# Kernel tuning notes

Hardware: AMD Instinct MI355X
Metric: run time of the kernel (lower is better)

The kernel has to match this reference:

```python
import jax, jax.numpy as jnp
import numpy as np

B, S, D = 1, 2048, 2048
HQ, HKV = 32, 8
HD = D // HQ          # 64
G = HQ // HKV         # 4 query heads per kv head


def apply_rope(x, freq):
    # x: (b, h, s, hd); freq: (s, hd//2) angles. Llama-style pairwise rotation.
    cos = jnp.cos(freq)  # (s, hd//2)
    sin = jnp.sin(freq)
    xr = x.reshape(*x.shape[:-1], HD // 2, 2)
    xe, xo = xr[..., 0], xr[..., 1]
    re = xe * cos - xo * sin
    ro = xe * sin + xo * cos
    return jnp.stack([re, ro], axis=-1).reshape(x.shape)


def setup_inputs() -> dict:
    key = jax.random.key(0)
    k1, k2, k3, k4, k5 = jax.random.split(key, 5)
    x = jax.random.normal(k1, (B, S, D), dtype=jnp.float32)
    # RoPE angles: pos * inv_freq, theta=10000
    inv_freq = 1.0 / (10000.0 ** (jnp.arange(0, HD, 2, dtype=jnp.float32) / HD))
    freq = jnp.arange(S, dtype=jnp.float32)[:, None] * inv_freq[None, :]  # (S, HD//2)
    mask = jnp.tril(jnp.ones((S, S), dtype=jnp.int32))
    scale = D ** -0.5
    wq = jax.random.normal(k2, (D, HQ * HD), dtype=jnp.float32) * scale
    wk = jax.random.normal(k3, (D, HKV * HD), dtype=jnp.float32) * scale
    wv = jax.random.normal(k4, (D, HKV * HD), dtype=jnp.float32) * scale
    wo = jax.random.normal(k5, (HQ * HD, D), dtype=jnp.float32) * scale
    return {"x": x, "freq": freq, "mask": mask, "wq": wq, "wk": wk, "wv": wv, "wo": wo}


def reference(x, freq, mask, wq, wk, wv, wo):
    b, s, d = x.shape
    q = (x @ wq).reshape(b, s, HQ, HD).transpose(0, 2, 1, 3)    # (b,HQ,s,hd)
    k = (x @ wk).reshape(b, s, HKV, HD).transpose(0, 2, 1, 3)   # (b,HKV,s,hd)
    v = (x @ wv).reshape(b, s, HKV, HD).transpose(0, 2, 1, 3)
    q = apply_rope(q, freq[:s])
    k = apply_rope(k, freq[:s])
    # GQA: broadcast kv heads over groups instead of repeat_interleave
    qg = q.reshape(b, HKV, G, s, HD)
    scores = jnp.einsum('bhgsd,bhtd->bhgst', qg, k)             # (b,HKV,G,s,s)
    scores = jnp.where(mask[:s, :s] == 0, -jnp.inf, scores)
    w = jax.nn.softmax(scores * (HD ** -0.5), axis=-1)
    out = jnp.einsum('bhgst,bhtd->bhgsd', w, v)
    out = out.reshape(b, HQ, s, HD).transpose(0, 2, 1, 3).reshape(b, s, HQ * HD)
    return out @ wo
```

## Files before the change

### kernel.cpp

```cpp
#include <hip/hip_runtime.h>

typedef unsigned short u16;
typedef unsigned int u32;
typedef unsigned long long u64;

using bf16x8 = __bf16 __attribute__((ext_vector_type(8)));
using f32x4  = float  __attribute__((ext_vector_type(4)));

#define LDS_SPACE __attribute__((address_space(3)))
#define GLB_SPACE __attribute__((address_space(1)))

static __device__ __forceinline__ u16 f2bf(float f) {
  union { float f; u32 u; } c; c.f = f;
  u32 u = c.u;
  return (u16)((u + 0x7fffu + ((u >> 16) & 1u)) >> 16);
}
static __device__ __forceinline__ float bf2f(u16 u) {
  union { u32 u; float f; } c; c.u = ((u32)u) << 16;
  return c.f;
}

static __device__ __forceinline__ void fence_barrier() {
  asm volatile("" ::: "memory");
  __builtin_amdgcn_s_barrier();
  asm volatile("" ::: "memory");
}

constexpr float SC = 0.18033688011112042f;

__global__ __launch_bounds__(256) void prep_k(const float* __restrict__ x,
                                              const float* __restrict__ wq,
                                              const float* __restrict__ wk,
                                              const float* __restrict__ wv,
                                              const float* __restrict__ wo,
                                              u16* __restrict__ x_bf,
                                              u16* __restrict__ wqkv_t,
                                              u16* __restrict__ wo_t) {
  const int b = blockIdx.x;
  if (b < 4096) {
    int i = b * 256 + threadIdx.x;
    float4 v = ((const float4*)x)[i];
    ushort4 o;
    o.x = f2bf(v.x); o.y = f2bf(v.y); o.z = f2bf(v.z); o.w = f2bf(v.w);
    ((ushort4*)x_bf)[i] = o;
    return;
  }
  const float* src; u16* dst; int C, bx, by; float scale = 1.0f;
  if (b < 8192)      { src = wq; dst = wqkv_t; C = 2048; int t = b - 4096; bx = t & 63; by = t >> 6; scale = SC; }
  else if (b < 9216) { src = wk; dst = wqkv_t + (size_t)2048 * 2048; C = 512; int t = b - 8192; bx = t & 15; by = t >> 4; }
  else if (b < 10240){ src = wv; dst = wqkv_t + (size_t)2560 * 2048; C = 512; int t = b - 9216; bx = t & 15; by = t >> 4; }
  else               { src = wo; dst = wo_t; C = 2048; int t = b - 10240; bx = t & 63; by = t >> 6; }
  __shared__ float t[32][33];
  const int lx = threadIdx.x & 31, ly = threadIdx.x >> 5;
  const int r0 = by * 32, c0 = bx * 32;
  #pragma unroll
  for (int i = 0; i < 32; i += 8)
    t[ly + i][lx] = src[(size_t)(r0 + ly + i) * C + c0 + lx];
  __syncthreads();
  #pragma unroll
  for (int i = 0; i < 32; i += 8)
    dst[(size_t)(c0 + ly + i) * 2048 + r0 + lx] = f2bf(t[lx][ly + i] * scale);
}

__global__ __launch_bounds__(256) void vtrans_k(const u16* __restrict__ Y,
                                                u16* __restrict__ Vt) {
  __shared__ u16 t[64][72];
  const int s0 = blockIdx.x * 64;
  const int c0 = blockIdx.y * 64;
  const int lx = threadIdx.x & 63, ly = threadIdx.x >> 6;
  #pragma unroll
  for (int i = 0; i < 64; i += 4)
    t[i + ly][lx] = Y[(size_t)(s0 + i + ly) * 3072 + 2560 + c0 + lx];
  __syncthreads();
  #pragma unroll
  for (int i = 0; i < 64; i += 4)
    Vt[(size_t)(c0 + i + ly) * 2048 + s0 + lx] = t[lx][i + ly];
}

template <typename OutT>
__global__ __launch_bounds__(256) void gemm64_k(const u16* __restrict__ A,
                                                const u16* __restrict__ Bt,
                                                OutT* __restrict__ C,
                                                int M, int N, int K) {
  __shared__ u16 As[2][64 * 64];
  __shared__ u16 Bs[2][128 * 64];
  const int tid = threadIdx.x, lane = tid & 63, w = tid >> 6;
  const int wr = w >> 1, wc = w & 1;
  const int bm = blockIdx.y, bn = blockIdx.x;
  const int l15 = lane & 15, lq = lane >> 4;
  f32x4 acc[2][4] = {};

  const int srow8 = lane >> 3;
  const int scolb = ((lane & 7) ^ srow8) * 16;
  const u16* AgR = A + (size_t)(bm * 64 + w * 16 + srow8) * K;
  const u16* BgR = Bt + (size_t)(bn * 128 + w * 32 + srow8) * K;

  auto stage = [&](int buf, int k0) {
    #pragma unroll
    for (int i = 0; i < 2; ++i)
      __builtin_amdgcn_global_load_lds(
          (const GLB_SPACE u32*)((const char*)(AgR + (size_t)i * 8 * K + k0) + scolb),
          (LDS_SPACE u32*)&As[buf][(w * 16 + i * 8) * 64], 16, 0, 0);
    #pragma unroll
    for (int i = 0; i < 4; ++i)
      __builtin_amdgcn_global_load_lds(
          (const GLB_SPACE u32*)((const char*)(BgR + (size_t)i * 8 * K + k0) + scolb),
          (LDS_SPACE u32*)&Bs[buf][(w * 32 + i * 8) * 64], 16, 0, 0);
  };

  stage(0, 0);
  for (int k0 = 0; k0 < K; k0 += 64) {
    const int cur = (k0 >> 6) & 1;
    fence_barrier();
    if (k0 + 64 < K) {
      stage(cur ^ 1, k0 + 64);
      asm volatile("s_waitcnt vmcnt(6)" ::: "memory");
    } else {
      asm volatile("s_waitcnt vmcnt(0)" ::: "memory");
    }
    fence_barrier();

    #pragma unroll
    for (int kk = 0; kk < 2; ++kk) {
      bf16x8 a[2], b[4];
      #pragma unroll
      for (int m = 0; m < 2; ++m) {
        const int ra = wr * 32 + m * 16 + l15;
        a[m] = *(const bf16x8*)&As[cur][ra * 64 + (((kk * 4 + lq) ^ (ra & 7)) << 3)];
      }
      #pragma unroll
      for (int n = 0; n < 4; ++n) {
        const int rb = wc * 64 + n * 16 + l15;
        b[n] = *(const bf16x8*)&Bs[cur][rb * 64 + (((kk * 4 + lq) ^ (rb & 7)) << 3)];
      }
      #pragma unroll
      for (int m = 0; m < 2; ++m)
        #pragma unroll
        for (int n = 0; n < 4; ++n)
          acc[m][n] = __builtin_amdgcn_mfma_f32_16x16x32_bf16(a[m], b[n], acc[m][n], 0, 0, 0);
    }
  }

  const int r0 = bm * 64 + wr * 32 + lq * 4;
  const int c0 = bn * 128 + wc * 64 + l15;
  #pragma unroll
  for (int m = 0; m < 2; ++m)
    #pragma unroll
    for (int n = 0; n < 4; ++n)
      #pragma unroll
      for (int r = 0; r < 4; ++r) {
        float v = acc[m][n][r];
        size_t off = (size_t)(r0 + m * 16 + r) * N + (c0 + n * 16);
        if constexpr (sizeof(OutT) == 2) ((u16*)C)[off] = f2bf(v);
        else C[off] = v;
      }
}

__global__ __launch_bounds__(256) void rope_k(u16* __restrict__ Y,
                                              const float* __restrict__ freq) {
  int idx = blockIdx.x * 256 + threadIdx.x;
  int s = idx / 1280;
  int rem = idx - s * 1280;
  int h = rem >> 5;
  int i = rem & 31;
  int col = (h < 32) ? (h * 64 + 2 * i) : (2048 + (h - 32) * 64 + 2 * i);
  float ang = freq[s * 32 + i];
  float sn, cs;
  sincosf(ang, &sn, &cs);
  size_t base = (size_t)s * 3072 + col;
  float e = bf2f(Y[base]), o = bf2f(Y[base + 1]);
  Y[base]     = f2bf(e * cs - o * sn);
  Y[base + 1] = f2bf(e * sn + o * cs);
}

__global__ __launch_bounds__(256, 3) void attn_part_k(const u16* __restrict__ Y,
                                                      const u16* __restrict__ Vtg,
                                                      u16* __restrict__ Opart,
                                                      float2* __restrict__ Ml,
                                                      u16* __restrict__ Out) {
  __shared__ u16 Ks[2][64 * 64];
  __shared__ u16 Vs[2][64 * 64];
  __shared__ u32 Ps[4][2][16 * 36];
  const int w = threadIdx.x >> 6, lane = threadIdx.x & 63;
  const int l15 = lane & 15, lq = lane >> 4;

  const int b = (int)blockIdx.x;
  const int head = b & 31;
  const int idx = b >> 5;
  const u64 tb = (idx < 12) ? 986161012810415591ULL : 1200400570313029ULL;
  const int v = (int)((tb >> ((idx < 12 ? idx : idx - 12) * 5)) & 31);
  const int qt = v & 15, ch = v >> 4;
  const int kvh = head >> 2;
  const int ntiles = 2 * qt + 2;
  const int half = qt + 1;
  const int tstart = ch ? half : 0;
  const int tend = (qt >= 8 && ch == 0) ? half : ntiles;
  const int q0w = qt * 128 + w * 32;

  const int srow = lane >> 3;
  const int scolb = ((lane & 7) ^ srow) * 16;
  auto stage = [&](int buf, int t) {
    const int t0 = t * 64;
    #pragma unroll
    for (int i = 0; i < 2; ++i) {
      const int r = w * 16 + i * 8;
      const char* gk = (const char*)(Y + (size_t)(t0 + r + srow) * 3072 + 2048 + kvh * 64) + scolb;
      __builtin_amdgcn_global_load_lds((const GLB_SPACE u32*)gk,
                                       (LDS_SPACE u32*)&Ks[buf][r * 64], 16, 0, 0);
      const char* gv = (const char*)(Vtg + (size_t)(kvh * 64 + r + srow) * 2048 + t0) + scolb;
      __builtin_amdgcn_global_load_lds((const GLB_SPACE u32*)gv,
                                       (LDS_SPACE u32*)&Vs[buf][r * 64], 16, 0, 0);
    }
  };

  stage(0, tstart);

  bf16x8 qf[2][2];
  #pragma unroll
  for (int qs = 0; qs < 2; ++qs)
    #pragma unroll
    for (int kk = 0; kk < 2; ++kk)
      qf[qs][kk] = *(const bf16x8*)&Y[(size_t)(q0w + qs * 16 + l15) * 3072 +
                                      head * 64 + kk * 32 + lq * 8];

  float m_[2] = { -1e30f, -1e30f };
  float l_[2] = { 0.f, 0.f };
  f32x4 accO[2][4] = {};

  for (int t = tstart; t < tend; ++t) {
    const int cur = (t - tstart) & 1;
    fence_barrier();
    if (t + 1 < tend) {
      stage(cur ^ 1, t + 1);
      asm volatile("s_waitcnt vmcnt(4)" ::: "memory");
    } else {
      asm volatile("s_waitcnt vmcnt(0)" ::: "memory");
    }
    fence_barrier();

    const int t0 = t * 64;
    if (t0 > q0w + 31) continue;

    const u16* Kb = Ks[cur];
    const u16* Vb = Vs[cur];

    f32x4 sc[2][4] = {};
    #pragma unroll
    for (int kk = 0; kk < 2; ++kk)
      #pragma unroll
      for (int kt = 0; kt < 4; ++kt) {
        const int rk = kt * 16 + l15;
        bf16x8 a = *(const bf16x8*)&Kb[rk * 64 + ((((kk * 4 + lq) ^ (rk & 7)) << 3))];
        sc[0][kt] = __builtin_amdgcn_mfma_f32_16x16x32_bf16(a, qf[0][kk], sc[0][kt], 0, 0, 0);
        sc[1][kt] = __builtin_amdgcn_mfma_f32_16x16x32_bf16(a, qf[1][kk], sc[1][kt], 0, 0, 0);
      }

    bf16x8 vf[2][4];
    #pragma unroll
    for (int c = 0; c < 2; ++c)
      #pragma unroll
      for (int dt = 0; dt < 4; ++dt) {
        const int rv = dt * 16 + l15;
        vf[c][dt] = *(const bf16x8*)&Vb[rv * 64 + ((((c * 4 + lq) ^ (rv & 7)) << 3))];
      }

    bool act[2];
    #pragma unroll
    for (int qs = 0; qs < 2; ++qs) {
      const int qsmin = q0w + qs * 16;
      act[qs] = (t0 <= qsmin + 15);
      if (!act[qs]) continue;
      const int qrow = qsmin + l15;
      if (t0 + 63 > qsmin) {
        #pragma unroll
        for (int n = 0; n < 4; ++n)
          #pragma unroll
          for (int rr = 0; rr < 4; ++rr)
            if (t0 + n * 16 + lq * 4 + rr > qrow) sc[qs][n][rr] = -1e30f;
      }
      float a0 = fmaxf(fmaxf(sc[qs][0][0], sc[qs][0][1]), fmaxf(sc[qs][0][2], sc[qs][0][3]));
      float a1 = fmaxf(fmaxf(sc[qs][1][0], sc[qs][1][1]), fmaxf(sc[qs][1][2], sc[qs][1][3]));
      float a2 = fmaxf(fmaxf(sc[qs][2][0], sc[qs][2][1]), fmaxf(sc[qs][2][2], sc[qs][2][3]));
      float a3 = fmaxf(fmaxf(sc[qs][3][0], sc[qs][3][1]), fmaxf(sc[qs][3][2], sc[qs][3][3]));
      float mx = fmaxf(fmaxf(a0, a1), fmaxf(a2, a3));

      if (__any(mx > m_[qs] + 7.25f)) {
        float mf = mx;
        mf = fmaxf(mf, __shfl_xor(mf, 16));
        mf = fmaxf(mf, __shfl_xor(mf, 32));
        const float mnew = fmaxf(m_[qs], mf);
        const float alpha = exp2f(m_[qs] - mnew);
        l_[qs] *= alpha;
        #pragma unroll
        for (int dt = 0; dt < 4; ++dt) accO[qs][dt] *= alpha;
        m_[qs] = mnew;
      }
      const float mS = m_[qs];
      float s0 = 0.f, s1 = 0.f, s2 = 0.f, s3 = 0.f;
      u64* pp = (u64*)&Ps[w][qs][l15 * 36 + lq * 2];
      #pragma unroll
      for (int n = 0; n < 4; ++n) {
        float p0 = exp2f(sc[qs][n][0] - mS);
        float p1 = exp2f(sc[qs][n][1] - mS);
        float p2 = exp2f(sc[qs][n][2] - mS);
        float p3 = exp2f(sc[qs][n][3] - mS);
        s0 += p0; s1 += p1; s2 += p2; s3 += p3;
        u32 w0, w1;
        asm("v_cvt_pk_bf16_f32 %0, %1, %2" : "=v"(w0) : "v"(p0), "v"(p1));
        asm("v_cvt_pk_bf16_f32 %0, %1, %2" : "=v"(w1) : "v"(p2), "v"(p3));
        pp[n * 4] = (u64)w0 | ((u64)w1 << 32);
      }
      l_[qs] += (s0 + s1) + (s2 + s3);
    }

    #pragma unroll
    for (int qs = 0; qs < 2; ++qs) {
      if (!act[qs]) continue;
      const u16* p16 = (const u16*)Ps[w][qs];
      #pragma unroll
      for (int c = 0; c < 2; ++c) {
        bf16x8 bb = *(const bf16x8*)&p16[l15 * 72 + c * 32 + lq * 8];
        #pragma unroll
        for (int dt = 0; dt < 4; ++dt)
          accO[qs][dt] = __builtin_amdgcn_mfma_f32_16x16x32_bf16(vf[c][dt], bb, accO[qs][dt], 0, 0, 0);
      }
    }
  }

  if (qt < 8) {
    #pragma unroll
    for (int qs = 0; qs < 2; ++qs) {
      float lt = l_[qs];
      lt += __shfl_xor(lt, 16);
      lt += __shfl_xor(lt, 32);
      const float rl = 1.0f / lt;
      const int qrow = q0w + qs * 16 + l15;
      #pragma unroll
      for (int dt = 0; dt < 4; ++dt) {
        ushort4 o;
        o.x = f2bf(accO[qs][dt][0] * rl);
        o.y = f2bf(accO[qs][dt][1] * rl);
        o.z = f2bf(accO[qs][dt][2] * rl);
        o.w = f2bf(accO[qs][dt][3] * rl);
        *(ushort4*)&Out[(size_t)qrow * 2048 + head * 64 + dt * 16 + lq * 4] = o;
      }
    }
    return;
  }

  const int slot = ((head << 3) + (qt - 8)) * 2 + ch;
  u16* ob = Opart + (size_t)slot * 8192;
  #pragma unroll
  for (int qs = 0; qs < 2; ++qs) {
    float lt = l_[qs];
    lt += __shfl_xor(lt, 16);
    lt += __shfl_xor(lt, 32);
    const int row = w * 32 + qs * 16 + l15;
    #pragma unroll
    for (int dt = 0; dt < 4; ++dt) {
      ushort4 o;
      o.x = f2bf(accO[qs][dt][0]);
      o.y = f2bf(accO[qs][dt][1]);
      o.z = f2bf(accO[qs][dt][2]);
      o.w = f2bf(accO[qs][dt][3]);
      *(ushort4*)&ob[row * 64 + dt * 16 + lq * 4] = o;
    }
    if (lq == 0) Ml[(size_t)slot * 128 + row] = make_float2(m_[qs], lt);
  }
}

__global__ __launch_bounds__(256) void attn_comb_k(const u16* __restrict__ Opart,
                                                   const float2* __restrict__ Ml,
                                                   u16* __restrict__ Out) {
  const int b = blockIdx.x;
  const int rg = b & 3;
  const int hq = b >> 2;
  const int head = hq >> 3;
  const int qt8 = hq & 7;
  const int slot0 = ((head << 3) + qt8) * 2;
  const int rl = threadIdx.x >> 3;
  const int d8 = (threadIdx.x & 7) * 8;
  const int row = rg * 32 + rl;

  float2 ml0 = Ml[(size_t)slot0 * 128 + row];
  float2 ml1 = Ml[(size_t)(slot0 + 1) * 128 + row];
  const float gm = fmaxf(ml0.x, ml1.x);
  const float a0 = exp2f(ml0.x - gm);
  const float a1 = exp2f(ml1.x - gm);
  const float rd = 1.0f / (a0 * ml0.y + a1 * ml1.y);

  const u16* p0 = &Opart[(size_t)slot0 * 8192 + row * 64 + d8];
  const u16* p1 = &Opart[(size_t)(slot0 + 1) * 8192 + row * 64 + d8];
  ushort4 q0 = *(const ushort4*)p0, q1 = *(const ushort4*)(p0 + 4);
  ushort4 r0 = *(const ushort4*)p1, r1 = *(const ushort4*)(p1 + 4);
  ushort4 o0, o1;
  o0.x = f2bf((a0 * bf2f(q0.x) + a1 * bf2f(r0.x)) * rd);
  o0.y = f2bf((a0 * bf2f(q0.y) + a1 * bf2f(r0.y)) * rd);
  o0.z = f2bf((a0 * bf2f(q0.z) + a1 * bf2f(r0.z)) * rd);
  o0.w = f2bf((a0 * bf2f(q0.w) + a1 * bf2f(r0.w)) * rd);
  o1.x = f2bf((a0 * bf2f(q1.x) + a1 * bf2f(r1.x)) * rd);
  o1.y = f2bf((a0 * bf2f(q1.y) + a1 * bf2f(r1.y)) * rd);
  o1.z = f2bf((a0 * bf2f(q1.z) + a1 * bf2f(r1.z)) * rd);
  o1.w = f2bf((a0 * bf2f(q1.w) + a1 * bf2f(r1.w)) * rd);
  u16* op = &Out[(size_t)((qt8 + 8) * 128 + row) * 2048 + head * 64 + d8];
  *(ushort4*)op = o0;
  *(ushort4*)(op + 4) = o1;
}

extern "C" void kernel_launch(void* const* d_in, const int* in_sizes, int n_in,
                              void* d_out, int out_size, void* d_ws, size_t ws_size,
                              hipStream_t stream) {
  const float* x    = (const float*)d_in[0];
  const float* freq = (const float*)d_in[1];
  const float* wq   = (const float*)d_in[3];
  const float* wk   = (const float*)d_in[4];
  const float* wv   = (const float*)d_in[5];
  const float* wo   = (const float*)d_in[6];
  float* out = (float*)d_out;

  u16* x_bf   = (u16*)d_ws;
  u16* wqkv_t = x_bf + (size_t)2048 * 2048;
  u16* wo_t   = wqkv_t + (size_t)3072 * 2048;
  u16* y      = wo_t + (size_t)2048 * 2048;
  u16* attn   = y + (size_t)2048 * 3072;
  u16* vt     = x_bf;
  u16* opart  = attn + (size_t)2048 * 2048;
  float2* ml  = (float2*)(opart + (size_t)512 * 8192);

  prep_k<<<14336, 256, 0, stream>>>(x, wq, wk, wv, wo, x_bf, wqkv_t, wo_t);
  gemm64_k<u16><<<dim3(24, 32), 256, 0, stream>>>(x_bf, wqkv_t, y, 2048, 3072, 2048);
  rope_k<<<10240, 256, 0, stream>>>(y, freq);
  vtrans_k<<<dim3(32, 8), 256, 0, stream>>>(y, vt);
  attn_part_k<<<768, 256, 0, stream>>>(y, vt, opart, ml, attn);
  attn_comb_k<<<1024, 256, 0, stream>>>(opart, ml, attn);
  gemm64_k<float><<<dim3(16, 32), 256, 0, stream>>>(attn, wo_t, out, 2048, 2048, 2048);
}
```

Before: 135.4 us.

## Shrink output GEMM tile, share swizzled P buffer, raise attention occupancy

The output-projection GEMM becomes templated on tile width and runs with 64-wide N tiles, doubling its grid from 512 to 1024 blocks so more CUs are busy. The attention kernel keeps one XOR-swizzled P staging buffer per wave instead of two padded ones, writing and consuming P inside the same per-subtile loop. Its launch bound goes from 3 to 4 blocks per SM, trading register headroom for occupancy. The smaller GEMM tile reuses each A tile across fewer columns, and the tighter register budget may cause spills.

```diff
diff --git a/kernel.cpp b/kernel.cpp
--- a/kernel.cpp
+++ b/kernel.cpp
@@ -77,23 +77,24 @@
     Vt[(size_t)(c0 + i + ly) * 2048 + s0 + lx] = t[lx][i + ly];
 }
 
-template <typename OutT>
+template <typename OutT, int BN>
 __global__ __launch_bounds__(256) void gemm64_k(const u16* __restrict__ A,
                                                 const u16* __restrict__ Bt,
                                                 OutT* __restrict__ C,
                                                 int M, int N, int K) {
+  constexpr int WN = BN / 32;
   __shared__ u16 As[2][64 * 64];
-  __shared__ u16 Bs[2][128 * 64];
+  __shared__ u16 Bs[2][BN * 64];
   const int tid = threadIdx.x, lane = tid & 63, w = tid >> 6;
   const int wr = w >> 1, wc = w & 1;
   const int bm = blockIdx.y, bn = blockIdx.x;
   const int l15 = lane & 15, lq = lane >> 4;
-  f32x4 acc[2][4] = {};
+  f32x4 acc[2][WN] = {};
 
   const int srow8 = lane >> 3;
   const int scolb = ((lane & 7) ^ srow8) * 16;
   const u16* AgR = A + (size_t)(bm * 64 + w * 16 + srow8) * K;
-  const u16* BgR = Bt + (size_t)(bn * 128 + w * 32 + srow8) * K;
+  const u16* BgR = Bt + (size_t)(bn * BN + w * (BN / 4) + srow8) * K;
 
   auto stage = [&](int buf, int k0) {
     #pragma unroll
@@ -102,10 +103,10 @@
           (const GLB_SPACE u32*)((const char*)(AgR + (size_t)i * 8 * K + k0) + scolb),
           (LDS_SPACE u32*)&As[buf][(w * 16 + i * 8) * 64], 16, 0, 0);
     #pragma unroll
-    for (int i = 0; i < 4; ++i)
+    for (int i = 0; i < WN; ++i)
       __builtin_amdgcn_global_load_lds(
           (const GLB_SPACE u32*)((const char*)(BgR + (size_t)i * 8 * K + k0) + scolb),
-          (LDS_SPACE u32*)&Bs[buf][(w * 32 + i * 8) * 64], 16, 0, 0);
+          (LDS_SPACE u32*)&Bs[buf][(w * (BN / 4) + i * 8) * 64], 16, 0, 0);
   };
 
   stage(0, 0);
@@ -114,7 +115,8 @@
     fence_barrier();
     if (k0 + 64 < K) {
       stage(cur ^ 1, k0 + 64);
-      asm volatile("s_waitcnt vmcnt(6)" ::: "memory");
+      if constexpr (BN == 128) asm volatile("s_waitcnt vmcnt(6)" ::: "memory");
+      else                     asm volatile("s_waitcnt vmcnt(4)" ::: "memory");
     } else {
       asm volatile("s_waitcnt vmcnt(0)" ::: "memory");
     }
@@ -122,31 +124,31 @@
 
     #pragma unroll
     for (int kk = 0; kk < 2; ++kk) {
-      bf16x8 a[2], b[4];
+      bf16x8 a[2], b[WN];
       #pragma unroll
       for (int m = 0; m < 2; ++m) {
         const int ra = wr * 32 + m * 16 + l15;
         a[m] = *(const bf16x8*)&As[cur][ra * 64 + (((kk * 4 + lq) ^ (ra & 7)) << 3)];
       }
       #pragma unroll
-      for (int n = 0; n < 4; ++n) {
-        const int rb = wc * 64 + n * 16 + l15;
+      for (int n = 0; n < WN; ++n) {
+        const int rb = wc * (BN / 2) + n * 16 + l15;
         b[n] = *(const bf16x8*)&Bs[cur][rb * 64 + (((kk * 4 + lq) ^ (rb & 7)) << 3)];
       }
       #pragma unroll
       for (int m = 0; m < 2; ++m)
         #pragma unroll
-        for (int n = 0; n < 4; ++n)
+        for (int n = 0; n < WN; ++n)
           acc[m][n] = __builtin_amdgcn_mfma_f32_16x16x32_bf16(a[m], b[n], acc[m][n], 0, 0, 0);
     }
   }
 
   const int r0 = bm * 64 + wr * 32 + lq * 4;
-  const int c0 = bn * 128 + wc * 64 + l15;
+  const int c0 = bn * BN + wc * (BN / 2) + l15;
   #pragma unroll
   for (int m = 0; m < 2; ++m)
     #pragma unroll
-    for (int n = 0; n < 4; ++n)
+    for (int n = 0; n < WN; ++n)
       #pragma unroll
       for (int r = 0; r < 4; ++r) {
         float v = acc[m][n][r];
@@ -173,14 +175,14 @@
   Y[base + 1] = f2bf(e * sn + o * cs);
 }
 
-__global__ __launch_bounds__(256, 3) void attn_part_k(const u16* __restrict__ Y,
+__global__ __launch_bounds__(256, 4) void attn_part_k(const u16* __restrict__ Y,
                                                       const u16* __restrict__ Vtg,
                                                       u16* __restrict__ Opart,
                                                       float2* __restrict__ Ml,
                                                       u16* __restrict__ Out) {
   __shared__ u16 Ks[2][64 * 64];
   __shared__ u16 Vs[2][64 * 64];
-  __shared__ u32 Ps[4][2][16 * 36];
+  __shared__ u32 Ps[4][16 * 32];
   const int w = threadIdx.x >> 6, lane = threadIdx.x & 63;
   const int l15 = lane & 15, lq = lane >> 4;
 
@@ -264,12 +266,10 @@
         vf[c][dt] = *(const bf16x8*)&Vb[rv * 64 + ((((c * 4 + lq) ^ (rv & 7)) << 3))];
       }
 
-    bool act[2];
     #pragma unroll
     for (int qs = 0; qs < 2; ++qs) {
       const int qsmin = q0w + qs * 16;
-      act[qs] = (t0 <= qsmin + 15);
-      if (!act[qs]) continue;
+      if (t0 > qsmin + 15) continue;
       const int qrow = qsmin + l15;
       if (t0 + 63 > qsmin) {
         #pragma unroll
@@ -297,7 +297,6 @@
       }
       const float mS = m_[qs];
       float s0 = 0.f, s1 = 0.f, s2 = 0.f, s3 = 0.f;
-      u64* pp = (u64*)&Ps[w][qs][l15 * 36 + lq * 2];
       #pragma unroll
       for (int n = 0; n < 4; ++n) {
         float p0 = exp2f(sc[qs][n][0] - mS);
@@ -308,18 +307,15 @@
         u32 w0, w1;
         asm("v_cvt_pk_bf16_f32 %0, %1, %2" : "=v"(w0) : "v"(p0), "v"(p1));
         asm("v_cvt_pk_bf16_f32 %0, %1, %2" : "=v"(w1) : "v"(p2), "v"(p3));
-        pp[n * 4] = (u64)w0 | ((u64)w1 << 32);
+        const u32 pidx = l15 * 32 + ((lq * 2 + n * 8) ^ ((l15 & 7) << 2));
+        *(u64*)&Ps[w][pidx] = (u64)w0 | ((u64)w1 << 32);
       }
       l_[qs] += (s0 + s1) + (s2 + s3);
-    }
-
-    #pragma unroll
-    for (int qs = 0; qs < 2; ++qs) {
-      if (!act[qs]) continue;
-      const u16* p16 = (const u16*)Ps[w][qs];
+
+      const u16* p16 = (const u16*)Ps[w];
       #pragma unroll
       for (int c = 0; c < 2; ++c) {
-        bf16x8 bb = *(const bf16x8*)&p16[l15 * 72 + c * 32 + lq * 8];
+        bf16x8 bb = *(const bf16x8*)&p16[l15 * 64 + ((c * 32 + lq * 8) ^ ((l15 & 7) << 3))];
         #pragma unroll
         for (int dt = 0; dt < 4; ++dt)
           accO[qs][dt] = __builtin_amdgcn_mfma_f32_16x16x32_bf16(vf[c][dt], bb, accO[qs][dt], 0, 0, 0);
@@ -428,10 +424,10 @@
   float2* ml  = (float2*)(opart + (size_t)512 * 8192);
 
   prep_k<<<14336, 256, 0, stream>>>(x, wq, wk, wv, wo, x_bf, wqkv_t, wo_t);
-  gemm64_k<u16><<<dim3(24, 32), 256, 0, stream>>>(x_bf, wqkv_t, y, 2048, 3072, 2048);
+  gemm64_k<u16, 128><<<dim3(24, 32), 256, 0, stream>>>(x_bf, wqkv_t, y, 2048, 3072, 2048);
   rope_k<<<10240, 256, 0, stream>>>(y, freq);
   vtrans_k<<<dim3(32, 8), 256, 0, stream>>>(y, vt);
   attn_part_k<<<768, 256, 0, stream>>>(y, vt, opart, ml, attn);
   attn_comb_k<<<1024, 256, 0, stream>>>(opart, ml, attn);
-  gemm64_k<float><<<dim3(16, 32), 256, 0, stream>>>(attn, wo_t, out, 2048, 2048, 2048);
-}
+  gemm64_k<float, 64><<<dim3(32, 32), 256, 0, stream>>>(attn, wo_t, out, 2048, 2048, 2048);
+}
```

After: 201.5 us. 1.49x slower.
